# Performance work log

Measured on AMD Instinct MI355X. Metric: run time of the kernel, lower is better.

The kernel has to match this reference:

```python
import jax, jax.numpy as jnp
import numpy as np

EMBED_DIM = 1024
NUM_HEADS = 16
BLOCK_SIZE = 128
GLOBAL_EVERY = 24


def make_block_sparse_mask(seq_len):
    # 0 where allowed, -inf where disallowed. Allowed iff same block, or
    # either position lies in a 'global' block (block index % global_every == 0).
    bi = jnp.arange(seq_len) // BLOCK_SIZE
    is_global = (bi % GLOBAL_EVERY) == 0
    allowed = (bi[:, None] == bi[None, :]) | is_global[:, None] | is_global[None, :]
    return jnp.where(allowed, 0.0, -jnp.inf).astype(jnp.float32)


def setup_inputs() -> dict:
    key = jax.random.key(0)
    k_x, k_w, k_wo = jax.random.split(key, 3)
    B, L, D = 1, 4096, EMBED_DIM
    x = jax.random.normal(k_x, (B, L, D), dtype=jnp.float32)
    # nn.MultiheadAttention params: packed in_proj [3D, D] + bias [3D], out_proj [D, D] + bias [D]
    w_qkv = jax.random.normal(k_w, (3 * D, D), dtype=jnp.float32) * 0.02
    b_qkv = jnp.zeros((3 * D,), dtype=jnp.float32)
    w_out = jax.random.normal(k_wo, (D, D), dtype=jnp.float32) * 0.02
    b_out = jnp.zeros((D,), dtype=jnp.float32)
    return {"x": x, "w_qkv": w_qkv, "b_qkv": b_qkv, "w_out": w_out, "b_out": b_out}


def reference(x, w_qkv, b_qkv, w_out, b_out):
    B, L, D = x.shape
    H = NUM_HEADS
    hd = D // H
    mask = make_block_sparse_mask(L)  # [L, L] additive
    qkv = x @ w_qkv.T + b_qkv  # [B, L, 3D]
    q, k, v = jnp.split(qkv, 3, axis=-1)
    # [B, H, L, hd]
    q = q.reshape(B, L, H, hd).transpose(0, 2, 1, 3)
    k = k.reshape(B, L, H, hd).transpose(0, 2, 1, 3)
    v = v.reshape(B, L, H, hd).transpose(0, 2, 1, 3)
    scale = 1.0 / jnp.sqrt(jnp.asarray(hd, dtype=x.dtype))
    scores = jnp.einsum('bhqd,bhkd->bhqk', q * scale, k) + mask  # [B, H, L, L]
    attn = jax.nn.softmax(scores, axis=-1)
    out = jnp.einsum('bhqk,bhkd->bhqd', attn, v)  # [B, H, L, hd]
    out = out.transpose(0, 2, 1, 3).reshape(B, L, D)
    return out @ w_out.T + b_out
```

## Files before the change

kernel.cpp:

```cpp
#include <hip/hip_runtime.h>
#include <hip/hip_bf16.h>
#include <math.h>


#define SEQ 4096
#define DIM 1024
#define NHEADS 16
#define HDIM 64
#define BS 128
#define PSTRIDE 136
#define ESTRIDE 136

using short8 = __attribute__((ext_vector_type(8))) short;
using floatx4 = __attribute__((ext_vector_type(4))) float;

__device__ __forceinline__ float bf2f(short s) {
  unsigned u = ((unsigned)(unsigned short)s) << 16;
  return __uint_as_float(u);
}

__device__ __forceinline__ void gld_lds16(const __hip_bfloat16* g, __hip_bfloat16* l) {
  __builtin_amdgcn_global_load_lds(
      (const __attribute__((address_space(1))) unsigned int*)g,
      (__attribute__((address_space(3))) unsigned int*)l, 16, 0, 0);
}

__global__ __launch_bounds__(256) void downcast3(
    const float* __restrict__ x, const float* __restrict__ wq,
    const float* __restrict__ wo, __hip_bfloat16* __restrict__ xd,
    __hip_bfloat16* __restrict__ wqd, __hip_bfloat16* __restrict__ wod) {
  int id = blockIdx.x;
  const float* src;
  __hip_bfloat16* dst;
  int base;
  if (id < 4096) { src = x; dst = xd; base = id; }
  else if (id < 7168) { src = wq; dst = wqd; base = id - 4096; }
  else { src = wo; dst = wod; base = id - 7168; }
  int i = (base * 256 + threadIdx.x) * 4;
  float4 v = *(const float4*)(src + i);
  __hip_bfloat16 b0 = __float2bfloat16(v.x);
  __hip_bfloat16 b1 = __float2bfloat16(v.y);
  __hip_bfloat16 b2 = __float2bfloat16(v.z);
  __hip_bfloat16 b3 = __float2bfloat16(v.w);
  ushort4 packed = {*(unsigned short*)&b0, *(unsigned short*)&b1,
                    *(unsigned short*)&b2, *(unsigned short*)&b3};
  *(ushort4*)(((unsigned short*)dst) + i) = packed;
}

__global__ __launch_bounds__(256) void gemm_qkv(const __hip_bfloat16* __restrict__ Amat,
                                                const __hip_bfloat16* __restrict__ Wmat,
                                                const float* __restrict__ Bias,
                                                __hip_bfloat16* __restrict__ qkv) {
  __shared__ __align__(16) char pool[128 * ESTRIDE * 2];
  __hip_bfloat16* Asmem = (__hip_bfloat16*)pool;
  __hip_bfloat16* Bsmem = (__hip_bfloat16*)(pool + 8192);
  __hip_bfloat16* Ep = (__hip_bfloat16*)pool;

  const int Kd = DIM;
  const int t = threadIdx.x;
  const int w = t >> 6;
  const int lane = t & 63;
  const int fr = lane & 15;
  const int quad = lane >> 4;
  const int wm = w >> 1, wn = w & 1;

  int id = blockIdx.x;
  int xcd = id & 7, j = id >> 3;
  int m_idx = xcd + (j & 3) * 8;
  int n_idx = j >> 2;
  const int m0 = m_idx * 128;
  const int n0 = n_idx * 128;
  const int s = n0 >> 10;
  const int cc0 = n0 & 1023;
  const bool vmode = (s == 2);

  const __hip_bfloat16* APtr = vmode ? Amat + (size_t)m0 * Kd : Wmat + (size_t)n0 * Kd;
  const __hip_bfloat16* BPtr = vmode ? Wmat + (size_t)n0 * Kd : Amat + (size_t)m0 * Kd;

  floatx4 acc[4][4];
#pragma unroll
  for (int i = 0; i < 4; ++i)
#pragma unroll
    for (int jj = 0; jj < 4; ++jj) acc[i][jj] = (floatx4){0.f, 0.f, 0.f, 0.f};

  for (int kk = 0; kk < Kd / 32; ++kk) {
#pragma unroll
    for (int jj = 0; jj < 2; ++jj) {
      int c = jj * 256 + t;
      int ldso = (jj * 256 + w * 64) * 8;
      gld_lds16(APtr + (size_t)(c >> 2) * Kd + kk * 32 + (c & 3) * 8, &Asmem[ldso]);
      gld_lds16(BPtr + (size_t)(c >> 2) * Kd + kk * 32 + (c & 3) * 8, &Bsmem[ldso]);
    }
    __syncthreads();
    short8 af[4], bf_[4];
#pragma unroll
    for (int mt = 0; mt < 4; ++mt)
      af[mt] = *(const short8*)&Asmem[(wm * 64 + mt * 16 + fr) * 32 + quad * 8];
#pragma unroll
    for (int nt = 0; nt < 4; ++nt)
      bf_[nt] = *(const short8*)&Bsmem[(wn * 64 + nt * 16 + fr) * 32 + quad * 8];
#pragma unroll
    for (int mt = 0; mt < 4; ++mt)
#pragma unroll
      for (int nt = 0; nt < 4; ++nt)
        acc[mt][nt] = __builtin_amdgcn_mfma_f32_16x16x32_bf16(af[mt], bf_[nt],
                                                              acc[mt][nt], 0, 0, 0);
    __syncthreads();
  }

#pragma unroll
  for (int nt = 0; nt < 4; ++nt) {
    int dcol = wn * 64 + nt * 16 + fr;
#pragma unroll
    for (int mt = 0; mt < 4; ++mt) {
      int drow0 = wm * 64 + mt * 16 + quad * 4;
      ushort4 pk;
      unsigned short* pks = (unsigned short*)&pk;
#pragma unroll
      for (int i = 0; i < 4; ++i) {
        __hip_bfloat16 bb = __float2bfloat16(acc[mt][nt][i]);
        pks[i] = *(unsigned short*)&bb;
      }
      *(ushort4*)&Ep[dcol * ESTRIDE + drow0] = pk;
    }
  }
  __syncthreads();

  if (!vmode) {
    __hip_bfloat16* dst = qkv + (size_t)s * SEQ * DIM;
#pragma unroll
    for (int rr = 0; rr < 8; ++rr) {
      int m = rr * 16 + (t >> 4);
      int ch = (t & 15) * 8;
      short8 v8 = *(const short8*)&Ep[m * ESTRIDE + ch];
      float4 b0 = *(const float4*)&Bias[n0 + ch];
      float4 b1 = *(const float4*)&Bias[n0 + ch + 4];
      float bb[8] = {b0.x, b0.y, b0.z, b0.w, b1.x, b1.y, b1.z, b1.w};
      short8 o8;
#pragma unroll
      for (int k = 0; k < 8; ++k) {
        __hip_bfloat16 ob = __float2bfloat16(bf2f(v8[k]) + bb[k]);
        o8[k] = *(short*)&ob;
      }
      *(short8*)&dst[(size_t)(m0 + m) * DIM + cc0 + ch] = o8;
    }
  } else {
    __hip_bfloat16* vt = qkv + 2ull * SEQ * DIM;
#pragma unroll
    for (int rr = 0; rr < 8; ++rr) {
      int nrow = rr * 16 + (t >> 4);
      int ch = (t & 15) * 8;
      float bv = Bias[n0 + nrow];
      short8 v8 = *(const short8*)&Ep[nrow * ESTRIDE + ch];
      short8 o8;
#pragma unroll
      for (int k = 0; k < 8; ++k) {
        __hip_bfloat16 ob = __float2bfloat16(bf2f(v8[k]) + bv);
        o8[k] = *(short*)&ob;
      }
      *(short8*)&vt[(size_t)(cc0 + nrow) * SEQ + m0 + ch] = o8;
    }
  }
}

__global__ __launch_bounds__(256) void gemm_out(const __hip_bfloat16* __restrict__ Amat,
                                                const __hip_bfloat16* __restrict__ Wmat,
                                                const float* __restrict__ Bias,
                                                float* __restrict__ out) {
  __shared__ __align__(16) __hip_bfloat16 Asmem[128 * 32];
  __shared__ __align__(16) __hip_bfloat16 Bsmem[128 * 32];
  const int Kd = DIM;
  const int t = threadIdx.x;
  const int w = t >> 6;
  const int lane = t & 63;
  const int fr = lane & 15;
  const int quad = lane >> 4;
  const int wm = w >> 1, wn = w & 1;
  int id = blockIdx.x;
  int xcd = id & 7, j = id >> 3;
  int m_idx = xcd + (j & 3) * 8;
  int n_idx = j >> 2;
  const int m0 = m_idx * 128;
  const int n0 = n_idx * 128;
  const __hip_bfloat16* Ablk = Amat + (size_t)m0 * Kd;
  const __hip_bfloat16* Bblk = Wmat + (size_t)n0 * Kd;
  floatx4 acc[4][4];
#pragma unroll
  for (int i = 0; i < 4; ++i)
#pragma unroll
    for (int jj = 0; jj < 4; ++jj) acc[i][jj] = (floatx4){0.f, 0.f, 0.f, 0.f};
  for (int kk = 0; kk < Kd / 32; ++kk) {
#pragma unroll
    for (int jj = 0; jj < 2; ++jj) {
      int c = jj * 256 + t;
      int ldso = (jj * 256 + w * 64) * 8;
      gld_lds16(Ablk + (size_t)(c >> 2) * Kd + kk * 32 + (c & 3) * 8, &Asmem[ldso]);
      gld_lds16(Bblk + (size_t)(c >> 2) * Kd + kk * 32 + (c & 3) * 8, &Bsmem[ldso]);
    }
    __syncthreads();
    short8 af[4], bf_[4];
#pragma unroll
    for (int mt = 0; mt < 4; ++mt)
      af[mt] = *(const short8*)&Asmem[(wm * 64 + mt * 16 + fr) * 32 + quad * 8];
#pragma unroll
    for (int nt = 0; nt < 4; ++nt)
      bf_[nt] = *(const short8*)&Bsmem[(wn * 64 + nt * 16 + fr) * 32 + quad * 8];
#pragma unroll
    for (int mt = 0; mt < 4; ++mt)
#pragma unroll
      for (int nt = 0; nt < 4; ++nt)
        acc[mt][nt] = __builtin_amdgcn_mfma_f32_16x16x32_bf16(af[mt], bf_[nt],
                                                              acc[mt][nt], 0, 0, 0);
    __syncthreads();
  }
#pragma unroll
  for (int nt = 0; nt < 4; ++nt) {
    int n = n0 + wn * 64 + nt * 16 + fr;
    float bv = Bias[n];
#pragma unroll
    for (int mt = 0; mt < 4; ++mt) {
      int m = m0 + wm * 64 + mt * 16 + quad * 4;
#pragma unroll
      for (int i = 0; i < 4; ++i)
        out[(size_t)(m + i) * DIM + n] = acc[mt][nt][i] + bv;
    }
  }
}

__global__ __launch_bounds__(256) void attn_mfma(
    const __hip_bfloat16* __restrict__ qkv,
    __hip_bfloat16* __restrict__ aout,
    float* __restrict__ po, float* __restrict__ pm, float* __restrict__ pl) {
  __shared__ __align__(16) __hip_bfloat16 Kbuf[16 * 512];
  __shared__ __align__(16) __hip_bfloat16 Vbuf[16 * 512];
  __shared__ __hip_bfloat16 p_lds[4 * 16 * PSTRIDE];
  const int h = blockIdx.y;
  const int wgid = blockIdx.x;
  const int t = threadIdx.x;
  const int wv = t >> 6;
  const int lane = t & 63;
  const int fr = lane & 15;
  const int quad = lane >> 4;

  int qb, q0, niter, slice = 0, pid = 0;
  bool direct;
  if (wgid < 60) {
    int nb = wgid >> 1;
    qb = (nb < 23) ? nb + 1 : nb + 2;
    q0 = qb * BS + (wgid & 1) * 64;
    niter = 3;
    direct = true;
  } else {
    int gi = wgid - 60;
    slice = gi & 7;
    int chunk = gi >> 3;
    qb = (chunk >> 1) * 24;
    q0 = qb * BS + (chunk & 1) * 64;
    niter = 4;
    direct = false;
    pid = (h * 4 + chunk) * 8 + slice;
  }

  const __hip_bfloat16* Q = qkv;
  const __hip_bfloat16* K = qkv + (size_t)SEQ * DIM;
  const __hip_bfloat16* Vt = qkv + 2ull * SEQ * DIM;

  short8 qa0, qa1;
  {
    const __hip_bfloat16* qp =
        Q + (size_t)(q0 + wv * 16 + fr) * DIM + h * HDIM + quad * 8;
    qa0 = *(const short8*)(qp);
    qa1 = *(const short8*)(qp + 32);
  }

  float mrow[4] = {-INFINITY, -INFINITY, -INFINITY, -INFINITY};
  float lsum[4] = {0.f, 0.f, 0.f, 0.f};
  floatx4 o[4];
#pragma unroll
  for (int i = 0; i < 4; ++i) o[i] = (floatx4){0.f, 0.f, 0.f, 0.f};

  __hip_bfloat16* pbase = &p_lds[wv * 16 * PSTRIDE];

  for (int bi = 0; bi < niter; ++bi) {
    int kb = direct ? (bi == 0 ? 0 : (bi == 1 ? qb : 24)) : slice * 4 + bi;

    const __hip_bfloat16* Kg = K + (size_t)(kb * BS) * DIM + h * HDIM;
    const __hip_bfloat16* Vg = Vt + (size_t)(h * HDIM) * SEQ + kb * BS;
    __syncthreads();
#pragma unroll
    for (int rr = 0; rr < 4; ++rr) {
      int f = rr * 4 + wv;
      int nt = f >> 1, ks = f & 1;
      gld_lds16(Kg + (size_t)(nt * 16 + fr) * DIM + ks * 32 + quad * 8,
                &Kbuf[f * 512]);
      int nt2 = f >> 2, ks2 = f & 3;
      gld_lds16(Vg + (size_t)(nt2 * 16 + fr) * SEQ + ks2 * 32 + quad * 8,
                &Vbuf[f * 512]);
    }
    __syncthreads();

    floatx4 s[8];
#pragma unroll
    for (int nt = 0; nt < 8; ++nt) {
      short8 kf0 = *(const short8*)&Kbuf[(nt * 2 + 0) * 512 + lane * 8];
      short8 kf1 = *(const short8*)&Kbuf[(nt * 2 + 1) * 512 + lane * 8];
      floatx4 acc = {0.f, 0.f, 0.f, 0.f};
      acc = __builtin_amdgcn_mfma_f32_16x16x32_bf16(qa0, kf0, acc, 0, 0, 0);
      acc = __builtin_amdgcn_mfma_f32_16x16x32_bf16(qa1, kf1, acc, 0, 0, 0);
      s[nt] = acc;
    }
#pragma unroll
    for (int nt = 0; nt < 8; ++nt)
#pragma unroll
      for (int i = 0; i < 4; ++i) s[nt][i] *= 0.125f;

    float rmax[4];
#pragma unroll
    for (int i = 0; i < 4; ++i) {
      float m = s[0][i];
#pragma unroll
      for (int nt = 1; nt < 8; ++nt) m = fmaxf(m, s[nt][i]);
      rmax[i] = m;
    }
#pragma unroll
    for (int off = 1; off < 16; off <<= 1)
#pragma unroll
      for (int i = 0; i < 4; ++i)
        rmax[i] = fmaxf(rmax[i], __shfl_xor(rmax[i], off, 64));

    float newm[4], alpha[4], psum[4];
#pragma unroll
    for (int i = 0; i < 4; ++i) {
      newm[i] = fmaxf(mrow[i], rmax[i]);
      alpha[i] = __expf(mrow[i] - newm[i]);
      psum[i] = 0.f;
    }
#pragma unroll
    for (int nt = 0; nt < 8; ++nt)
#pragma unroll
      for (int i = 0; i < 4; ++i) {
        float p = __expf(s[nt][i] - newm[i]);
        psum[i] += p;
        __hip_bfloat16 pb = __float2bfloat16(p);
        pbase[(quad * 4 + i) * PSTRIDE + nt * 16 + fr] = pb;
      }
#pragma unroll
    for (int off = 1; off < 16; off <<= 1)
#pragma unroll
      for (int i = 0; i < 4; ++i) psum[i] += __shfl_xor(psum[i], off, 64);
#pragma unroll
    for (int i = 0; i < 4; ++i) {
      lsum[i] = lsum[i] * alpha[i] + psum[i];
      mrow[i] = newm[i];
    }
#pragma unroll
    for (int nt2 = 0; nt2 < 4; ++nt2)
#pragma unroll
      for (int i = 0; i < 4; ++i) o[nt2][i] *= alpha[i];

    short8 ap[4];
#pragma unroll
    for (int ks2 = 0; ks2 < 4; ++ks2)
      ap[ks2] = *(const short8*)&pbase[fr * PSTRIDE + ks2 * 32 + quad * 8];

#pragma unroll
    for (int nt2 = 0; nt2 < 4; ++nt2) {
#pragma unroll
      for (int ks2 = 0; ks2 < 4; ++ks2) {
        short8 vb = *(const short8*)&Vbuf[(nt2 * 4 + ks2) * 512 + lane * 8];
        o[nt2] = __builtin_amdgcn_mfma_f32_16x16x32_bf16(ap[ks2], vb, o[nt2], 0, 0, 0);
      }
    }
  }

  if (direct) {
    float inv[4];
#pragma unroll
    for (int i = 0; i < 4; ++i) inv[i] = 1.f / lsum[i];
#pragma unroll
    for (int nt2 = 0; nt2 < 4; ++nt2)
#pragma unroll
      for (int i = 0; i < 4; ++i)
        aout[(size_t)(q0 + wv * 16 + quad * 4 + i) * DIM + h * HDIM + nt2 * 16 + fr] =
            __float2bfloat16(o[nt2][i] * inv[i]);
  } else {
    float* pob = po + (size_t)pid * 4096 + (wv * 16 + quad * 4) * 64 + fr;
#pragma unroll
    for (int nt2 = 0; nt2 < 4; ++nt2)
#pragma unroll
      for (int i = 0; i < 4; ++i) pob[i * 64 + nt2 * 16] = o[nt2][i];
    if (fr == 0) {
#pragma unroll
      for (int i = 0; i < 4; ++i) {
        pm[pid * 64 + wv * 16 + quad * 4 + i] = mrow[i];
        pl[pid * 64 + wv * 16 + quad * 4 + i] = lsum[i];
      }
    }
  }
}

__global__ __launch_bounds__(256) void combine(const float* __restrict__ po,
                                               const float* __restrict__ pm,
                                               const float* __restrict__ pl,
                                               __hip_bfloat16* __restrict__ aout) {
  int b = blockIdx.x;
  int h = b >> 2, chunk = b & 3;
  int t = threadIdx.x;
  int row = t >> 2;
  int d0 = (t & 3) * 16;

  float m8[8];
  float newm = -INFINITY;
#pragma unroll
  for (int s = 0; s < 8; ++s) {
    m8[s] = pm[(b * 8 + s) * 64 + row];
    newm = fmaxf(newm, m8[s]);
  }
  float wgt[8], lsum = 0.f;
#pragma unroll
  for (int s = 0; s < 8; ++s) {
    wgt[s] = __expf(m8[s] - newm);
    lsum += pl[(b * 8 + s) * 64 + row] * wgt[s];
  }
  float acc[16];
#pragma unroll
  for (int jj = 0; jj < 16; ++jj) acc[jj] = 0.f;
#pragma unroll
  for (int s = 0; s < 8; ++s) {
    const float* src = po + ((size_t)(b * 8 + s) * 4096) + row * 64 + d0;
#pragma unroll
    for (int j4 = 0; j4 < 4; ++j4) {
      float4 v = *(const float4*)(src + j4 * 4);
      acc[j4 * 4 + 0] += wgt[s] * v.x;
      acc[j4 * 4 + 1] += wgt[s] * v.y;
      acc[j4 * 4 + 2] += wgt[s] * v.z;
      acc[j4 * 4 + 3] += wgt[s] * v.w;
    }
  }
  float inv = 1.f / lsum;
  int qrow = (chunk >> 1) * 3072 + (chunk & 1) * 64 + row;
#pragma unroll
  for (int jj = 0; jj < 16; ++jj)
    aout[(size_t)qrow * DIM + h * HDIM + d0 + jj] = __float2bfloat16(acc[jj] * inv);
}

extern "C" void kernel_launch(void* const* d_in, const int* in_sizes, int n_in,
                              void* d_out, int out_size, void* d_ws, size_t ws_size,
                              hipStream_t stream) {
  const float* x = (const float*)d_in[0];
  const float* w_qkv = (const float*)d_in[1];
  const float* b_qkv = (const float*)d_in[2];
  const float* w_out = (const float*)d_in[3];
  const float* b_out = (const float*)d_in[4];
  float* out = (float*)d_out;

  char* wsb = (char*)d_ws;
  __hip_bfloat16* qkv_ws = (__hip_bfloat16*)(wsb);
  __hip_bfloat16* x_bf = (__hip_bfloat16*)(wsb + 24ull * 1024 * 1024);
  __hip_bfloat16* wqkv_bf = (__hip_bfloat16*)(wsb + 32ull * 1024 * 1024);
  __hip_bfloat16* wout_bf = (__hip_bfloat16*)(wsb + 38ull * 1024 * 1024);
  __hip_bfloat16* attn_ws = (__hip_bfloat16*)(wsb + 40ull * 1024 * 1024);
  float* po = (float*)(wsb + 24ull * 1024 * 1024);
  float* pm = (float*)(wsb + 32ull * 1024 * 1024);
  float* pl = (float*)(wsb + 32ull * 1024 * 1024 + 131072);

  dim3 blk(256);
  downcast3<<<dim3(8192), blk, 0, stream>>>(x, w_qkv, w_out, x_bf, wqkv_bf, wout_bf);
  gemm_qkv<<<dim3(768), blk, 0, stream>>>(x_bf, wqkv_bf, b_qkv, qkv_ws);
  attn_mfma<<<dim3(92, NHEADS), blk, 0, stream>>>(qkv_ws, attn_ws, po, pm, pl);
  combine<<<dim3(64), blk, 0, stream>>>(po, pm, pl, attn_ws);
  gemm_out<<<dim3(256), blk, 0, stream>>>(attn_ws, wout_bf, b_out, out);
}
```

Baseline: 178.1 us.

## Transpose attention score MFMA to keep P in registers; halve gemm_out N tile

The attention kernel swaps the MFMA operand order so each lane holds a whole query row's scores. The row max and sum then need only two cross-lane shuffles, and P is packed to bf16 and redistributed with shuffles instead of a round trip through LDS. Output and partial stores become vectorized. Separately, gemm_out uses 128x64 tiles with 512 blocks, raising occupancy on the 256-CU device at the cost of more reloads of A.

```diff
diff --git a/kernel.cpp b/kernel.cpp
--- a/kernel.cpp
+++ b/kernel.cpp
@@ -8,7 +8,6 @@
 #define NHEADS 16
 #define HDIM 64
 #define BS 128
-#define PSTRIDE 136
 #define ESTRIDE 136
 
 using short8 = __attribute__((ext_vector_type(8))) short;
@@ -17,6 +16,12 @@
 __device__ __forceinline__ float bf2f(short s) {
   unsigned u = ((unsigned)(unsigned short)s) << 16;
   return __uint_as_float(u);
+}
+
+__device__ __forceinline__ unsigned pack_bf16(float a, float b) {
+  __hip_bfloat16 ba = __float2bfloat16(a);
+  __hip_bfloat16 bb = __float2bfloat16(b);
+  return ((unsigned)*(unsigned short*)&bb << 16) | (unsigned)*(unsigned short*)&ba;
 }
 
 __device__ __forceinline__ void gld_lds16(const __hip_bfloat16* g, __hip_bfloat16* l) {
@@ -168,7 +173,7 @@
                                                 const float* __restrict__ Bias,
                                                 float* __restrict__ out) {
   __shared__ __align__(16) __hip_bfloat16 Asmem[128 * 32];
-  __shared__ __align__(16) __hip_bfloat16 Bsmem[128 * 32];
+  __shared__ __align__(16) __hip_bfloat16 Bsmem[64 * 32];
   const int Kd = DIM;
   const int t = threadIdx.x;
   const int w = t >> 6;
@@ -181,41 +186,41 @@
   int m_idx = xcd + (j & 3) * 8;
   int n_idx = j >> 2;
   const int m0 = m_idx * 128;
-  const int n0 = n_idx * 128;
+  const int n0 = n_idx * 64;
   const __hip_bfloat16* Ablk = Amat + (size_t)m0 * Kd;
   const __hip_bfloat16* Bblk = Wmat + (size_t)n0 * Kd;
-  floatx4 acc[4][4];
+  floatx4 acc[4][2];
 #pragma unroll
   for (int i = 0; i < 4; ++i)
 #pragma unroll
-    for (int jj = 0; jj < 4; ++jj) acc[i][jj] = (floatx4){0.f, 0.f, 0.f, 0.f};
+    for (int jj = 0; jj < 2; ++jj) acc[i][jj] = (floatx4){0.f, 0.f, 0.f, 0.f};
   for (int kk = 0; kk < Kd / 32; ++kk) {
 #pragma unroll
     for (int jj = 0; jj < 2; ++jj) {
       int c = jj * 256 + t;
       int ldso = (jj * 256 + w * 64) * 8;
       gld_lds16(Ablk + (size_t)(c >> 2) * Kd + kk * 32 + (c & 3) * 8, &Asmem[ldso]);
-      gld_lds16(Bblk + (size_t)(c >> 2) * Kd + kk * 32 + (c & 3) * 8, &Bsmem[ldso]);
-    }
-    __syncthreads();
-    short8 af[4], bf_[4];
+    }
+    gld_lds16(Bblk + (size_t)(t >> 2) * Kd + kk * 32 + (t & 3) * 8, &Bsmem[t * 8]);
+    __syncthreads();
+    short8 af[4], bf_[2];
 #pragma unroll
     for (int mt = 0; mt < 4; ++mt)
       af[mt] = *(const short8*)&Asmem[(wm * 64 + mt * 16 + fr) * 32 + quad * 8];
 #pragma unroll
-    for (int nt = 0; nt < 4; ++nt)
-      bf_[nt] = *(const short8*)&Bsmem[(wn * 64 + nt * 16 + fr) * 32 + quad * 8];
+    for (int nt = 0; nt < 2; ++nt)
+      bf_[nt] = *(const short8*)&Bsmem[(wn * 32 + nt * 16 + fr) * 32 + quad * 8];
 #pragma unroll
     for (int mt = 0; mt < 4; ++mt)
 #pragma unroll
-      for (int nt = 0; nt < 4; ++nt)
+      for (int nt = 0; nt < 2; ++nt)
         acc[mt][nt] = __builtin_amdgcn_mfma_f32_16x16x32_bf16(af[mt], bf_[nt],
                                                               acc[mt][nt], 0, 0, 0);
     __syncthreads();
   }
 #pragma unroll
-  for (int nt = 0; nt < 4; ++nt) {
-    int n = n0 + wn * 64 + nt * 16 + fr;
+  for (int nt = 0; nt < 2; ++nt) {
+    int n = n0 + wn * 32 + nt * 16 + fr;
     float bv = Bias[n];
 #pragma unroll
     for (int mt = 0; mt < 4; ++mt) {
@@ -233,7 +238,6 @@
     float* __restrict__ po, float* __restrict__ pm, float* __restrict__ pl) {
   __shared__ __align__(16) __hip_bfloat16 Kbuf[16 * 512];
   __shared__ __align__(16) __hip_bfloat16 Vbuf[16 * 512];
-  __shared__ __hip_bfloat16 p_lds[4 * 16 * PSTRIDE];
   const int h = blockIdx.y;
   const int wgid = blockIdx.x;
   const int t = threadIdx.x;
@@ -273,13 +277,10 @@
     qa1 = *(const short8*)(qp + 32);
   }
 
-  float mrow[4] = {-INFINITY, -INFINITY, -INFINITY, -INFINITY};
-  float lsum[4] = {0.f, 0.f, 0.f, 0.f};
+  float mrow = -INFINITY, lsum = 0.f;
   floatx4 o[4];
 #pragma unroll
   for (int i = 0; i < 4; ++i) o[i] = (floatx4){0.f, 0.f, 0.f, 0.f};
-
-  __hip_bfloat16* pbase = &p_lds[wv * 16 * PSTRIDE];
 
   for (int bi = 0; bi < niter; ++bi) {
     int kb = direct ? (bi == 0 ? 0 : (bi == 1 ? qb : 24)) : slice * 4 + bi;
@@ -305,8 +306,8 @@
       short8 kf0 = *(const short8*)&Kbuf[(nt * 2 + 0) * 512 + lane * 8];
       short8 kf1 = *(const short8*)&Kbuf[(nt * 2 + 1) * 512 + lane * 8];
       floatx4 acc = {0.f, 0.f, 0.f, 0.f};
-      acc = __builtin_amdgcn_mfma_f32_16x16x32_bf16(qa0, kf0, acc, 0, 0, 0);
-      acc = __builtin_amdgcn_mfma_f32_16x16x32_bf16(qa1, kf1, acc, 0, 0, 0);
+      acc = __builtin_amdgcn_mfma_f32_16x16x32_bf16(kf0, qa0, acc, 0, 0, 0);
+      acc = __builtin_amdgcn_mfma_f32_16x16x32_bf16(kf1, qa1, acc, 0, 0, 0);
       s[nt] = acc;
     }
 #pragma unroll
@@ -314,87 +315,82 @@
 #pragma unroll
       for (int i = 0; i < 4; ++i) s[nt][i] *= 0.125f;
 
-    float rmax[4];
-#pragma unroll
-    for (int i = 0; i < 4; ++i) {
-      float m = s[0][i];
-#pragma unroll
-      for (int nt = 1; nt < 8; ++nt) m = fmaxf(m, s[nt][i]);
-      rmax[i] = m;
-    }
-#pragma unroll
-    for (int off = 1; off < 16; off <<= 1)
-#pragma unroll
-      for (int i = 0; i < 4; ++i)
-        rmax[i] = fmaxf(rmax[i], __shfl_xor(rmax[i], off, 64));
-
-    float newm[4], alpha[4], psum[4];
-#pragma unroll
-    for (int i = 0; i < 4; ++i) {
-      newm[i] = fmaxf(mrow[i], rmax[i]);
-      alpha[i] = __expf(mrow[i] - newm[i]);
-      psum[i] = 0.f;
-    }
+    float rmax = -INFINITY;
 #pragma unroll
     for (int nt = 0; nt < 8; ++nt)
 #pragma unroll
-      for (int i = 0; i < 4; ++i) {
-        float p = __expf(s[nt][i] - newm[i]);
-        psum[i] += p;
-        __hip_bfloat16 pb = __float2bfloat16(p);
-        pbase[(quad * 4 + i) * PSTRIDE + nt * 16 + fr] = pb;
-      }
-#pragma unroll
-    for (int off = 1; off < 16; off <<= 1)
-#pragma unroll
-      for (int i = 0; i < 4; ++i) psum[i] += __shfl_xor(psum[i], off, 64);
-#pragma unroll
-    for (int i = 0; i < 4; ++i) {
-      lsum[i] = lsum[i] * alpha[i] + psum[i];
-      mrow[i] = newm[i];
-    }
+      for (int i = 0; i < 4; ++i) rmax = fmaxf(rmax, s[nt][i]);
+    rmax = fmaxf(rmax, __shfl_xor(rmax, 16, 64));
+    rmax = fmaxf(rmax, __shfl_xor(rmax, 32, 64));
+    float newm = fmaxf(mrow, rmax);
+    float alpha = __expf(mrow - newm);
+    float psum = 0.f;
+    unsigned pki[8][2];
+#pragma unroll
+    for (int nt = 0; nt < 8; ++nt) {
+      float p0 = __expf(s[nt][0] - newm);
+      float p1 = __expf(s[nt][1] - newm);
+      float p2 = __expf(s[nt][2] - newm);
+      float p3 = __expf(s[nt][3] - newm);
+      psum += (p0 + p1) + (p2 + p3);
+      pki[nt][0] = pack_bf16(p0, p1);
+      pki[nt][1] = pack_bf16(p2, p3);
+    }
+    psum += __shfl_xor(psum, 16, 64);
+    psum += __shfl_xor(psum, 32, 64);
+    lsum = lsum * alpha + psum;
+    mrow = newm;
 #pragma unroll
     for (int nt2 = 0; nt2 < 4; ++nt2)
 #pragma unroll
-      for (int i = 0; i < 4; ++i) o[nt2][i] *= alpha[i];
-
-    short8 ap[4];
-#pragma unroll
-    for (int ks2 = 0; ks2 < 4; ++ks2)
-      ap[ks2] = *(const short8*)&pbase[fr * PSTRIDE + ks2 * 32 + quad * 8];
+      for (int i = 0; i < 4; ++i) o[nt2][i] *= alpha;
+
+    union { int w4[4]; short8 s8; } pw[4];
+#pragma unroll
+    for (int ks2 = 0; ks2 < 4; ++ks2) {
+#pragma unroll
+      for (int p = 0; p < 4; ++p) {
+        int srcl = fr + ((((quad & 1) << 1) + (p >> 1)) << 4);
+        int lo = __shfl((int)pki[2 * ks2][p & 1], srcl, 64);
+        int hi = __shfl((int)pki[2 * ks2 + 1][p & 1], srcl, 64);
+        pw[ks2].w4[p] = (quad & 2) ? hi : lo;
+      }
+    }
 
 #pragma unroll
     for (int nt2 = 0; nt2 < 4; ++nt2) {
 #pragma unroll
       for (int ks2 = 0; ks2 < 4; ++ks2) {
         short8 vb = *(const short8*)&Vbuf[(nt2 * 4 + ks2) * 512 + lane * 8];
-        o[nt2] = __builtin_amdgcn_mfma_f32_16x16x32_bf16(ap[ks2], vb, o[nt2], 0, 0, 0);
+        o[nt2] = __builtin_amdgcn_mfma_f32_16x16x32_bf16(vb, pw[ks2].s8, o[nt2], 0, 0, 0);
       }
     }
   }
 
   if (direct) {
-    float inv[4];
-#pragma unroll
-    for (int i = 0; i < 4; ++i) inv[i] = 1.f / lsum[i];
-#pragma unroll
-    for (int nt2 = 0; nt2 < 4; ++nt2)
-#pragma unroll
-      for (int i = 0; i < 4; ++i)
-        aout[(size_t)(q0 + wv * 16 + quad * 4 + i) * DIM + h * HDIM + nt2 * 16 + fr] =
-            __float2bfloat16(o[nt2][i] * inv[i]);
+    float inv = 1.f / lsum;
+    __hip_bfloat16* orow = aout + (size_t)(q0 + wv * 16 + fr) * DIM + h * HDIM + quad * 4;
+#pragma unroll
+    for (int nt2 = 0; nt2 < 4; ++nt2) {
+      ushort4 pk;
+      unsigned short* pks = (unsigned short*)&pk;
+#pragma unroll
+      for (int i = 0; i < 4; ++i) {
+        __hip_bfloat16 ob = __float2bfloat16(o[nt2][i] * inv);
+        pks[i] = *(unsigned short*)&ob;
+      }
+      *(ushort4*)(orow + nt2 * 16) = pk;
+    }
   } else {
-    float* pob = po + (size_t)pid * 4096 + (wv * 16 + quad * 4) * 64 + fr;
-#pragma unroll
-    for (int nt2 = 0; nt2 < 4; ++nt2)
-#pragma unroll
-      for (int i = 0; i < 4; ++i) pob[i * 64 + nt2 * 16] = o[nt2][i];
-    if (fr == 0) {
-#pragma unroll
-      for (int i = 0; i < 4; ++i) {
-        pm[pid * 64 + wv * 16 + quad * 4 + i] = mrow[i];
-        pl[pid * 64 + wv * 16 + quad * 4 + i] = lsum[i];
-      }
+    float* pob = po + (size_t)pid * 4096 + (wv * 16 + fr) * 64 + quad * 4;
+#pragma unroll
+    for (int nt2 = 0; nt2 < 4; ++nt2) {
+      float4 v = {o[nt2][0], o[nt2][1], o[nt2][2], o[nt2][3]};
+      *(float4*)(pob + nt2 * 16) = v;
+    }
+    if (quad == 0) {
+      pm[pid * 64 + wv * 16 + fr] = mrow;
+      pl[pid * 64 + wv * 16 + fr] = lsum;
     }
   }
 }
@@ -469,5 +465,5 @@
   gemm_qkv<<<dim3(768), blk, 0, stream>>>(x_bf, wqkv_bf, b_qkv, qkv_ws);
   attn_mfma<<<dim3(92, NHEADS), blk, 0, stream>>>(qkv_ws, attn_ws, po, pm, pl);
   combine<<<dim3(64), blk, 0, stream>>>(po, pm, pl, attn_ws);
-  gemm_out<<<dim3(256), blk, 0, stream>>>(attn_ws, wout_bf, b_out, out);
-}
+  gemm_out<<<dim3(512), blk, 0, stream>>>(attn_ws, wout_bf, b_out, out);
+}
```

Result: faster. 174.5 us (-2.0%).
